# Optimization experiments

Hardware: AMD Instinct MI355X
Metric: run time of the kernel (lower is better)

## Reference

```python
import jax, jax.numpy as jnp
import numpy as np

D_MODEL = 768
MIMO_RANK = 4


def setup_inputs() -> dict:
    key = jax.random.key(0)
    ks = jax.random.split(key, 6)
    B, T, D, R = 2, 2048, D_MODEL, MIMO_RANK
    x = jax.random.normal(ks[0], (B, T, D), dtype=jnp.float32)
    norm_w = jnp.ones((D,), dtype=jnp.float32)
    W_in = jax.random.normal(ks[1], (D * R * 2, D), dtype=jnp.float32) * 0.02
    W_out = jax.random.normal(ks[2], (D, D), dtype=jnp.float32) * 0.02
    a_param = jax.random.normal(ks[3], (D, R, 2), dtype=jnp.float32) * 0.12
    b_param = jax.random.normal(ks[4], (D, R, 2), dtype=jnp.float32) * 0.15
    c_param = jax.random.normal(ks[5], (D, R, 2), dtype=jnp.float32) * 0.15
    return {"x": x, "norm_w": norm_w, "W_in": W_in, "W_out": W_out,
            "a_param": a_param, "b_param": b_param, "c_param": c_param}


def reference(x, norm_w, W_in, W_out, a_param, b_param, c_param):
    B, T, D = x.shape
    R = a_param.shape[1]
    # RMSNorm
    xn = x * jax.lax.rsqrt(jnp.mean(x * x, axis=-1, keepdims=True) + 1e-6) * norm_w
    # in_proj -> interleaved complex MIMO input u: [B,T,D,R,2]
    u = (xn @ W_in.T).reshape(B, T, D, R, 2)
    # coefficients (tanh-bounded; |a| scaled by 0.97 for stability)
    a = jnp.tanh(a_param) * 0.97
    b = jnp.tanh(b_param)
    c = jnp.tanh(c_param)
    ac = jax.lax.complex(a[..., 0], a[..., 1])  # [D,R]
    bc = jax.lax.complex(b[..., 0], b[..., 1])
    cc = jax.lax.complex(c[..., 0], c[..., 1])
    uc = jax.lax.complex(u[..., 0], u[..., 1])  # [B,T,D,R]
    # linear complex recurrence s_t = a * s_{t-1} + b * u_t, zero init state,
    # parallelized with an associative scan over time.
    bu = bc[None, None] * uc
    A = jnp.broadcast_to(ac[None, None], bu.shape)

    def comb(l, r):
        return (l[0] * r[0], r[0] * l[1] + r[1])

    _, s = jax.lax.associative_scan(comb, (A, bu), axis=1)  # [B,T,D,R] complex
    # output mix: real part of c * h, summed over MIMO rank -> [B,T,D]
    y = jnp.real(cc[None, None] * s).sum(axis=-1)
    return y @ W_out.T
```

## Files before the change

kernel.cpp:

```cpp
#include <hip/hip_runtime.h>
#include <hip/hip_bf16.h>
#include <stdint.h>

#define BATCH 2
#define TT 2048
#define DM 768
#define RR 4
#define M_TOK 4096
#define NFEAT 6144
#define NCH 6144
#define CHUNK 64
#define NCHUNK 32

typedef __attribute__((ext_vector_type(8))) short short8;
typedef __attribute__((ext_vector_type(4))) float float4v;

__device__ inline float bf2f(uint32_t bits16) {
    union { uint32_t u; float f; } x; x.u = bits16 << 16; return x.f;
}

typedef const __attribute__((address_space(1))) void* gptr_t;
typedef __attribute__((address_space(3))) void* lptr_t;

__device__ inline void async_ld16(const void* g, void* l) {
    __builtin_amdgcn_global_load_lds((gptr_t)(uintptr_t)g, (lptr_t)(uintptr_t)l,
                                     16, 0, 0);
}

__device__ inline void store_c(__hip_bfloat16* C, size_t idx, float v) {
    C[idx] = __float2bfloat16(v);
}
__device__ inline void store_c(float* C, size_t idx, float v) { C[idx] = v; }

__device__ inline uint2 pack4bf(float a, float b, float c, float d) {
    union { __hip_bfloat16 h[4]; uint2 u; } o;
    o.h[0] = __float2bfloat16(a); o.h[1] = __float2bfloat16(b);
    o.h[2] = __float2bfloat16(c); o.h[3] = __float2bfloat16(d);
    return o.u;
}

__device__ inline uint32_t pack2bf(float a, float b) {
    union { __hip_bfloat16 h[2]; uint32_t u; } o;
    o.h[0] = __float2bfloat16(a); o.h[1] = __float2bfloat16(b);
    return o.u;
}

__device__ inline float2 cmul(float2 a, float2 b) {
    return make_float2(a.x * b.x - a.y * b.y, a.x * b.y + a.y * b.x);
}

__device__ inline void cstep(float& sr, float& si, float2 a, float2 bb,
                             uint32_t uw) {
    float ur = bf2f(uw & 0xffffu), ui = bf2f(uw >> 16);
    float tr = bb.x * ur - bb.y * ui;
    float ti = bb.x * ui + bb.y * ur;
    float nr = a.x * sr - a.y * si + tr;
    float ni = a.x * si + a.y * sr + ti;
    sr = nr; si = ni;
}

__global__ __launch_bounds__(256) void prep_rms(
    const float* __restrict__ x, const float* __restrict__ w,
    const float* __restrict__ W_in, const float* __restrict__ W_out,
    const float* __restrict__ ap, const float* __restrict__ bp,
    const float* __restrict__ cp,
    __hip_bfloat16* __restrict__ xn,
    __hip_bfloat16* __restrict__ Win_bf, __hip_bfloat16* __restrict__ Wout_bf,
    float2* __restrict__ ac, float2* __restrict__ bc,
    float2* __restrict__ cc, float2* __restrict__ aQ,
    float2* __restrict__ aL) {
    int bid = blockIdx.x;
    int tid = threadIdx.x;
    if (bid < M_TOK) {
        __shared__ float wsum[3];
        float4 v = make_float4(0.f, 0.f, 0.f, 0.f);
        if (tid < 192) v = ((const float4*)(x + (size_t)bid * DM))[tid];
        float ss = v.x * v.x + v.y * v.y + v.z * v.z + v.w * v.w;
        #pragma unroll
        for (int o = 1; o < 64; o <<= 1) ss += __shfl_xor(ss, o);
        if (tid < 192 && (tid & 63) == 0) wsum[tid >> 6] = ss;
        __syncthreads();
        if (tid < 192) {
            float tot = wsum[0] + wsum[1] + wsum[2];
            float scale = rsqrtf(tot * (1.f / DM) + 1e-6f);
            float4 wv = ((const float4*)w)[tid];
            ((uint2*)(xn + (size_t)bid * DM))[tid] =
                pack4bf(v.x * scale * wv.x, v.y * scale * wv.y,
                        v.z * scale * wv.z, v.w * scale * wv.w);
        }
        return;
    }
    const int N1 = NFEAT * DM / 4;
    const int N2 = DM * DM / 4;
    int i = (bid - M_TOK) * 256 + tid;
    if (i < N1) {
        float4 v = ((const float4*)W_in)[i];
        ((uint2*)Win_bf)[i] = pack4bf(v.x, v.y, v.z, v.w);
    } else if (i < N1 + N2) {
        int k = i - N1;
        float4 v = ((const float4*)W_out)[k];
        ((uint2*)Wout_bf)[k] = pack4bf(v.x, v.y, v.z, v.w);
    }
    if (i < DM * RR) {
        float ar = tanhf(ap[2 * i])     * 0.97f;
        float ai = tanhf(ap[2 * i + 1]) * 0.97f;
        ac[i] = make_float2(ar, ai);
        bc[i] = make_float2(tanhf(bp[2 * i]), tanhf(bp[2 * i + 1]));
        cc[i] = make_float2(tanhf(cp[2 * i]), tanhf(cp[2 * i + 1]));
        float xr = ar, xi = ai;
        #pragma unroll
        for (int k = 0; k < 4; ++k) {
            float nr = xr * xr - xi * xi;
            float ni = 2.f * xr * xi;
            xr = nr; xi = ni;
        }
        aQ[i] = make_float2(xr, xi);
        #pragma unroll
        for (int k = 0; k < 2; ++k) {
            float nr = xr * xr - xi * xi;
            float ni = 2.f * xr * xi;
            xr = nr; xi = ni;
        }
        aL[i] = make_float2(xr, xi);
    }
}

template <int BM, int BN, int BK, typename OutT>
__device__ inline void gemm_body(
    const __hip_bfloat16* __restrict__ A, const __hip_bfloat16* __restrict__ B,
    OutT* __restrict__ C, int K, int ldc) {
    constexpr int MI = BM / 32;
    constexpr int NJ = BN / 32;
    constexpr int CPR = BK / 8;
    __shared__ __attribute__((aligned(16))) __hip_bfloat16 lA[BM * BK];
    __shared__ __attribute__((aligned(16))) __hip_bfloat16 lB[BN * BK];
    const int tid  = threadIdx.x;
    const int lane = tid & 63;
    const int wave = tid >> 6;
    const int quad = lane >> 4;
    const int l15  = lane & 15;
    const int wm = (wave >> 1) * (BM / 2);
    const int wn = (wave & 1) * (BN / 2);
    const int m0 = blockIdx.y * BM;
    const int n0 = blockIdx.x * BN;

    float4v acc[MI][NJ] = {};

    for (int k0 = 0; k0 < K; k0 += BK) {
        __syncthreads();
        #pragma unroll
        for (int it = 0; it < BM * CPR / 256; ++it) {
            int p = it * 256 + tid;
            int row = p / CPR;
            int cg = (p & (CPR - 1)) ^ (row & (CPR - 1));
            async_ld16(A + (size_t)(m0 + row) * K + k0 + cg * 8, lA + p * 8);
        }
        #pragma unroll
        for (int it = 0; it < BN * CPR / 256; ++it) {
            int p = it * 256 + tid;
            int row = p / CPR;
            int cg = (p & (CPR - 1)) ^ (row & (CPR - 1));
            async_ld16(B + (size_t)(n0 + row) * K + k0 + cg * 8, lB + p * 8);
        }
        __syncthreads();
        #pragma unroll
        for (int s = 0; s < BK / 32; ++s) {
            short8 af[MI], bfr[NJ];
            #pragma unroll
            for (int i = 0; i < MI; ++i) {
                int r = wm + i * 16 + l15;
                int c = (s * 4 + quad) ^ (r & (CPR - 1));
                af[i] = *(const short8*)(lA + r * BK + c * 8);
            }
            #pragma unroll
            for (int j = 0; j < NJ; ++j) {
                int r = wn + j * 16 + l15;
                int c = (s * 4 + quad) ^ (r & (CPR - 1));
                bfr[j] = *(const short8*)(lB + r * BK + c * 8);
            }
            #pragma unroll
            for (int i = 0; i < MI; ++i)
                #pragma unroll
                for (int j = 0; j < NJ; ++j)
                    acc[i][j] = __builtin_amdgcn_mfma_f32_16x16x32_bf16(
                        af[i], bfr[j], acc[i][j], 0, 0, 0);
        }
    }
    #pragma unroll
    for (int i = 0; i < MI; ++i)
        #pragma unroll
        for (int j = 0; j < NJ; ++j)
            #pragma unroll
            for (int rg = 0; rg < 4; ++rg) {
                int row = m0 + wm + i * 16 + quad * 4 + rg;
                int col = n0 + wn + j * 16 + l15;
                store_c(C, (size_t)row * ldc + col, acc[i][j][rg]);
            }
}

__global__ __launch_bounds__(256) void gemm_out(
    const __hip_bfloat16* __restrict__ A, const __hip_bfloat16* __restrict__ B,
    float* __restrict__ C, int K) {
    gemm_body<64, 64, 128, float>(A, B, C, K, DM);
}

__global__ __launch_bounds__(256) void gemm_in_scan(
    const __hip_bfloat16* __restrict__ A,
    const __hip_bfloat16* __restrict__ B,
    const float2* __restrict__ ac, const float2* __restrict__ bc,
    const float2* __restrict__ cc,
    __hip_bfloat16* __restrict__ y_local,
    float2* __restrict__ chunkEnd) {
    constexpr int BM = 128, BN = 128, BK = 64;
    constexpr int MI = BM / 32, NJ = BN / 32, CPR = BK / 8;
    constexpr int K = DM;
    __shared__ __attribute__((aligned(16))) __hip_bfloat16 smem[BM * BK + BN * BK];
    __hip_bfloat16* lA = smem;
    __hip_bfloat16* lB = smem + BM * BK;
    const int tid  = threadIdx.x;
    const int lane = tid & 63;
    const int wave = tid >> 6;
    const int quad = lane >> 4;
    const int l15  = lane & 15;
    const int wm = (wave >> 1) * (BM / 2);
    const int wn = (wave & 1) * (BN / 2);
    const int m0 = blockIdx.y * BM;
    const int n0 = blockIdx.x * BN;

    float4v acc[MI][NJ] = {};

    for (int k0 = 0; k0 < K; k0 += BK) {
        __syncthreads();
        #pragma unroll
        for (int it = 0; it < BM * CPR / 256; ++it) {
            int p = it * 256 + tid;
            int row = p / CPR;
            int cg = (p & (CPR - 1)) ^ (row & (CPR - 1));
            async_ld16(A + (size_t)(m0 + row) * K + k0 + cg * 8, lA + p * 8);
        }
        #pragma unroll
        for (int it = 0; it < BN * CPR / 256; ++it) {
            int p = it * 256 + tid;
            int row = p / CPR;
            int cg = (p & (CPR - 1)) ^ (row & (CPR - 1));
            async_ld16(B + (size_t)(n0 + row) * K + k0 + cg * 8, lB + p * 8);
        }
        __syncthreads();
        #pragma unroll
        for (int s = 0; s < BK / 32; ++s) {
            short8 af[MI], bfr[NJ];
            #pragma unroll
            for (int i = 0; i < MI; ++i) {
                int r = wm + i * 16 + l15;
                int c = (s * 4 + quad) ^ (r & (CPR - 1));
                af[i] = *(const short8*)(lA + r * BK + c * 8);
            }
            #pragma unroll
            for (int j = 0; j < NJ; ++j) {
                int r = wn + j * 16 + l15;
                int c = (s * 4 + quad) ^ (r & (CPR - 1));
                bfr[j] = *(const short8*)(lB + r * BK + c * 8);
            }
            #pragma unroll
            for (int i = 0; i < MI; ++i)
                #pragma unroll
                for (int j = 0; j < NJ; ++j)
                    acc[i][j] = __builtin_amdgcn_mfma_f32_16x16x32_bf16(
                        af[i], bfr[j], acc[i][j], 0, 0, 0);
        }
    }

    __syncthreads();
    uint32_t* up = (uint32_t*)smem;
    #pragma unroll
    for (int i = 0; i < MI; ++i)
        #pragma unroll
        for (int j = 0; j < NJ; ++j) {
            float s0 = __shfl_xor(acc[i][j][0], 1);
            float s1 = __shfl_xor(acc[i][j][1], 1);
            float s2 = __shfl_xor(acc[i][j][2], 1);
            float s3 = __shfl_xor(acc[i][j][3], 1);
            const bool odd = l15 & 1;
            float lo0 = odd ? s2 : acc[i][j][0];
            float hi0 = odd ? acc[i][j][2] : s0;
            float lo1 = odd ? s3 : acc[i][j][1];
            float hi1 = odd ? acc[i][j][3] : s1;
            int row0 = wm + i * 16 + quad * 4 + (odd ? 2 : 0);
            int row1 = row0 + 1;
            int pr = (wn + j * 16 + (l15 & ~1)) >> 1;
            int sl = pr & 3;
            up[row0 * 64 + (((pr >> 2) ^ (row0 & 15)) << 2) + sl] =
                pack2bf(lo0, hi0);
            up[row1 * 64 + (((pr >> 2) ^ (row1 & 15)) << 2) + sl] =
                pack2bf(lo1, hi1);
        }
    __syncthreads();

    if (tid < 32) {
        const int d_loc = tid & 15;
        const int half  = tid >> 4;
        const int d_g   = (n0 >> 3) + d_loc;
        const int cb    = d_g * RR;
        float2 a0 = ac[cb], a1 = ac[cb + 1], a2 = ac[cb + 2], a3 = ac[cb + 3];
        float2 b0 = bc[cb], b1 = bc[cb + 1], b2 = bc[cb + 2], b3 = bc[cb + 3];
        float2 c0 = cc[cb], c1 = cc[cb + 1], c2 = cc[cb + 2], c3 = cc[cb + 3];
        const int bb = m0 >> 11;
        const int j  = ((m0 & (TT - 1)) >> 6) + half;
        const uint4* up4 = (const uint4*)smem;
        float s0r = 0, s0i = 0, s1r = 0, s1i = 0;
        float s2r = 0, s2i = 0, s3r = 0, s3i = 0;
        size_t ybase = (size_t)(m0 + half * 64) * DM + d_g;
        #pragma unroll 4
        for (int t = 0; t < CHUNK; ++t) {
            int row = half * 64 + t;
            uint4 uw = up4[row * 16 + (d_loc ^ (row & 15))];
            cstep(s0r, s0i, a0, b0, uw.x);
            cstep(s1r, s1i, a1, b1, uw.y);
            cstep(s2r, s2i, a2, b2, uw.z);
            cstep(s3r, s3i, a3, b3, uw.w);
            float yv = c0.x * s0r - c0.y * s0i + c1.x * s1r - c1.y * s1i
                     + c2.x * s2r - c2.y * s2i + c3.x * s3r - c3.y * s3i;
            y_local[ybase + (size_t)t * DM] = __float2bfloat16(yv);
        }
        size_t eb = (size_t)j * NCH + bb * (DM * RR) + cb;
        chunkEnd[eb]     = make_float2(s0r, s0i);
        chunkEnd[eb + 1] = make_float2(s1r, s1i);
        chunkEnd[eb + 2] = make_float2(s2r, s2i);
        chunkEnd[eb + 3] = make_float2(s3r, s3i);
    }
}

__global__ __launch_bounds__(256) void scan_fix(
    const __hip_bfloat16* __restrict__ y_local,
    const float2* __restrict__ ac, const float2* __restrict__ cc,
    const float2* __restrict__ aQp, const float2* __restrict__ aLp,
    const float2* __restrict__ chunkEnd,
    __hip_bfloat16* __restrict__ y) {
    int g = blockIdx.x * 256 + threadIdx.x;
    int j = blockIdx.y;
    int z = blockIdx.z;
    int b = g >= DM;
    int d = g - b * DM;
    int cb = d * RR;
    float2 a0 = ac[cb], a1 = ac[cb + 1], a2 = ac[cb + 2], a3 = ac[cb + 3];
    float2 aL0 = aLp[cb], aL1 = aLp[cb + 1], aL2 = aLp[cb + 2], aL3 = aLp[cb + 3];
    float2 k0 = make_float2(0, 0), k1 = k0, k2 = k0, k3 = k0;
    for (int jj = 0; jj < j; ++jj) {
        size_t eb = (size_t)jj * NCH + b * (DM * RR) + cb;
        float2 e0 = chunkEnd[eb],     e1 = chunkEnd[eb + 1];
        float2 e2 = chunkEnd[eb + 2], e3 = chunkEnd[eb + 3];
        float nr, ni;
        nr = aL0.x * k0.x - aL0.y * k0.y + e0.x; ni = aL0.x * k0.y + aL0.y * k0.x + e0.y; k0 = make_float2(nr, ni);
        nr = aL1.x * k1.x - aL1.y * k1.y + e1.x; ni = aL1.x * k1.y + aL1.y * k1.x + e1.y; k1 = make_float2(nr, ni);
        nr = aL2.x * k2.x - aL2.y * k2.y + e2.x; ni = aL2.x * k2.y + aL2.y * k2.x + e2.y; k2 = make_float2(nr, ni);
        nr = aL3.x * k3.x - aL3.y * k3.y + e3.x; ni = aL3.x * k3.y + aL3.y * k3.x + e3.y; k3 = make_float2(nr, ni);
    }
    float2 q0 = cmul(cmul(cc[cb],     k0), a0);
    float2 q1 = cmul(cmul(cc[cb + 1], k1), a1);
    float2 q2 = cmul(cmul(cc[cb + 2], k2), a2);
    float2 q3 = cmul(cmul(cc[cb + 3], k3), a3);
    float2 aQ0 = aQp[cb], aQ1 = aQp[cb + 1], aQ2 = aQp[cb + 2], aQ3 = aQp[cb + 3];
    for (int zz = 0; zz < z; ++zz) {
        q0 = cmul(q0, aQ0); q1 = cmul(q1, aQ1);
        q2 = cmul(q2, aQ2); q3 = cmul(q3, aQ3);
    }
    size_t base = ((size_t)(b * TT + j * CHUNK + z * 16)) * DM + d;
    #pragma unroll 4
    for (int i = 0; i < 16; ++i) {
        float yv = bf2f(((const uint16_t*)y_local)[base + (size_t)i * DM])
                 + q0.x + q1.x + q2.x + q3.x;
        y[base + (size_t)i * DM] = __float2bfloat16(yv);
        q0 = cmul(q0, a0); q1 = cmul(q1, a1);
        q2 = cmul(q2, a2); q3 = cmul(q3, a3);
    }
}

extern "C" void kernel_launch(void* const* d_in, const int* in_sizes, int n_in,
                              void* d_out, int out_size, void* d_ws,
                              size_t ws_size, hipStream_t stream) {
    const float* x      = (const float*)d_in[0];
    const float* norm_w = (const float*)d_in[1];
    const float* W_in   = (const float*)d_in[2];
    const float* W_out  = (const float*)d_in[3];
    const float* a_p    = (const float*)d_in[4];
    const float* b_p    = (const float*)d_in[5];
    const float* c_p    = (const float*)d_in[6];
    float* out = (float*)d_out;

    char* ws = (char*)d_ws;
    size_t off = 0;
    auto alloc = [&](size_t bytes) {
        void* p = ws + off;
        off += (bytes + 255) & ~(size_t)255;
        return p;
    };
    __hip_bfloat16* Win_bf  = (__hip_bfloat16*)alloc((size_t)NFEAT * DM * 2);
    __hip_bfloat16* Wout_bf = (__hip_bfloat16*)alloc((size_t)DM * DM * 2);
    __hip_bfloat16* xn      = (__hip_bfloat16*)alloc((size_t)M_TOK * DM * 2);
    __hip_bfloat16* y_local = (__hip_bfloat16*)alloc((size_t)M_TOK * DM * 2);
    __hip_bfloat16* y       = (__hip_bfloat16*)alloc((size_t)M_TOK * DM * 2);
    float2* ac = (float2*)alloc((size_t)DM * RR * 8);
    float2* bc = (float2*)alloc((size_t)DM * RR * 8);
    float2* cc = (float2*)alloc((size_t)DM * RR * 8);
    float2* aQ = (float2*)alloc((size_t)DM * RR * 8);
    float2* aL = (float2*)alloc((size_t)DM * RR * 8);
    float2* chunkEnd = (float2*)alloc((size_t)NCHUNK * NCH * 8);

    {
        int cast_blocks = ((NFEAT * DM + DM * DM) / 4 + 255) / 256;
        prep_rms<<<M_TOK + cast_blocks, 256, 0, stream>>>(
            x, norm_w, W_in, W_out, a_p, b_p, c_p,
            xn, Win_bf, Wout_bf, ac, bc, cc, aQ, aL);
    }
    gemm_in_scan<<<dim3(NFEAT / 128, M_TOK / 128), 256, 0, stream>>>(
        xn, Win_bf, ac, bc, cc, y_local, chunkEnd);
    scan_fix<<<dim3(BATCH * DM / 256, NCHUNK, 4), 256, 0, stream>>>(
        y_local, ac, cc, aQ, aL, chunkEnd, y);
    gemm_out<<<dim3(DM / 64, M_TOK / 64), 256, 0, stream>>>(
        y, Wout_bf, out, DM);
}
```

Before: 198.7 us.

## Parallelize in-block chunk scan across all threads and pack RMSNorm per wave

The fused GEMM+scan epilogue previously ran the 64-step recurrence on only 32 threads. Now all 256 threads each scan 8 timesteps, exchange sub-chunk end states through extra shared memory, and combine them with a^8 carries before writing outputs. The LDS swizzle is changed to avoid bank conflicts for the new access pattern. RMSNorm now processes four tokens per block, one per wave, with no shared-memory reduction. The cost is extra LDS, another barrier, and a short serial carry loop per thread.

```diff
diff --git a/kernel.cpp b/kernel.cpp
--- a/kernel.cpp
+++ b/kernel.cpp
@@ -47,6 +47,13 @@
 
 __device__ inline float2 cmul(float2 a, float2 b) {
     return make_float2(a.x * b.x - a.y * b.y, a.x * b.y + a.y * b.x);
+}
+__device__ inline float2 cmad(float2 a, float2 b, float2 c) {
+    return make_float2(a.x * b.x - a.y * b.y + c.x,
+                       a.x * b.y + a.y * b.x + c.y);
+}
+__device__ inline float2 csq(float2 a) {
+    return make_float2(a.x * a.x - a.y * a.y, 2.f * a.x * a.y);
 }
 
 __device__ inline void cstep(float& sr, float& si, float2 a, float2 bb,
@@ -71,28 +78,32 @@
     float2* __restrict__ aL) {
     int bid = blockIdx.x;
     int tid = threadIdx.x;
-    if (bid < M_TOK) {
-        __shared__ float wsum[3];
-        float4 v = make_float4(0.f, 0.f, 0.f, 0.f);
-        if (tid < 192) v = ((const float4*)(x + (size_t)bid * DM))[tid];
-        float ss = v.x * v.x + v.y * v.y + v.z * v.z + v.w * v.w;
+    const int RMS_BLOCKS = M_TOK / 4;
+    if (bid < RMS_BLOCKS) {
+        int lane = tid & 63;
+        int token = bid * 4 + (tid >> 6);
+        const float4* xr = (const float4*)(x + (size_t)token * DM);
+        float4 v0 = xr[lane], v1 = xr[lane + 64], v2 = xr[lane + 128];
+        float ss = v0.x * v0.x + v0.y * v0.y + v0.z * v0.z + v0.w * v0.w
+                 + v1.x * v1.x + v1.y * v1.y + v1.z * v1.z + v1.w * v1.w
+                 + v2.x * v2.x + v2.y * v2.y + v2.z * v2.z + v2.w * v2.w;
         #pragma unroll
         for (int o = 1; o < 64; o <<= 1) ss += __shfl_xor(ss, o);
-        if (tid < 192 && (tid & 63) == 0) wsum[tid >> 6] = ss;
-        __syncthreads();
-        if (tid < 192) {
-            float tot = wsum[0] + wsum[1] + wsum[2];
-            float scale = rsqrtf(tot * (1.f / DM) + 1e-6f);
-            float4 wv = ((const float4*)w)[tid];
-            ((uint2*)(xn + (size_t)bid * DM))[tid] =
-                pack4bf(v.x * scale * wv.x, v.y * scale * wv.y,
-                        v.z * scale * wv.z, v.w * scale * wv.w);
-        }
+        float scale = rsqrtf(ss * (1.f / DM) + 1e-6f);
+        const float4* wr = (const float4*)w;
+        float4 w0 = wr[lane], w1 = wr[lane + 64], w2 = wr[lane + 128];
+        uint2* o = (uint2*)(xn + (size_t)token * DM);
+        o[lane] = pack4bf(v0.x * scale * w0.x, v0.y * scale * w0.y,
+                          v0.z * scale * w0.z, v0.w * scale * w0.w);
+        o[lane + 64] = pack4bf(v1.x * scale * w1.x, v1.y * scale * w1.y,
+                               v1.z * scale * w1.z, v1.w * scale * w1.w);
+        o[lane + 128] = pack4bf(v2.x * scale * w2.x, v2.y * scale * w2.y,
+                                v2.z * scale * w2.z, v2.w * scale * w2.w);
         return;
     }
     const int N1 = NFEAT * DM / 4;
     const int N2 = DM * DM / 4;
-    int i = (bid - M_TOK) * 256 + tid;
+    int i = (bid - RMS_BLOCKS) * 256 + tid;
     if (i < N1) {
         float4 v = ((const float4*)W_in)[i];
         ((uint2*)Win_bf)[i] = pack4bf(v.x, v.y, v.z, v.w);
@@ -214,7 +225,8 @@
     constexpr int BM = 128, BN = 128, BK = 64;
     constexpr int MI = BM / 32, NJ = BN / 32, CPR = BK / 8;
     constexpr int K = DM;
-    __shared__ __attribute__((aligned(16))) __hip_bfloat16 smem[BM * BK + BN * BK];
+    __shared__ __attribute__((aligned(16))) __hip_bfloat16
+        smem[BM * BK + BN * BK + 4096];
     __hip_bfloat16* lA = smem;
     __hip_bfloat16* lB = smem + BM * BK;
     const int tid  = threadIdx.x;
@@ -289,44 +301,78 @@
             int row1 = row0 + 1;
             int pr = (wn + j * 16 + (l15 & ~1)) >> 1;
             int sl = pr & 3;
-            up[row0 * 64 + (((pr >> 2) ^ (row0 & 15)) << 2) + sl] =
-                pack2bf(lo0, hi0);
-            up[row1 * 64 + (((pr >> 2) ^ (row1 & 15)) << 2) + sl] =
-                pack2bf(lo1, hi1);
+            int ch0 = (pr >> 2) ^ ((row0 ^ (row0 >> 2)) & 15);
+            int ch1 = (pr >> 2) ^ ((row1 ^ (row1 >> 2)) & 15);
+            up[row0 * 64 + ch0 * 4 + sl] = pack2bf(lo0, hi0);
+            up[row1 * 64 + ch1 * 4 + sl] = pack2bf(lo1, hi1);
         }
     __syncthreads();
 
-    if (tid < 32) {
+    {
         const int d_loc = tid & 15;
-        const int half  = tid >> 4;
+        const int s8    = (tid >> 4) & 7;
+        const int half  = tid >> 7;
         const int d_g   = (n0 >> 3) + d_loc;
         const int cb    = d_g * RR;
         float2 a0 = ac[cb], a1 = ac[cb + 1], a2 = ac[cb + 2], a3 = ac[cb + 3];
         float2 b0 = bc[cb], b1 = bc[cb + 1], b2 = bc[cb + 2], b3 = bc[cb + 3];
         float2 c0 = cc[cb], c1 = cc[cb + 1], c2 = cc[cb + 2], c3 = cc[cb + 3];
-        const int bb = m0 >> 11;
-        const int j  = ((m0 & (TT - 1)) >> 6) + half;
         const uint4* up4 = (const uint4*)smem;
+        float2* se = (float2*)(smem + (BM * BK + BN * BK));
+        const int rbase = half * 64 + s8 * 8;
+
         float s0r = 0, s0i = 0, s1r = 0, s1i = 0;
         float s2r = 0, s2i = 0, s3r = 0, s3i = 0;
-        size_t ybase = (size_t)(m0 + half * 64) * DM + d_g;
-        #pragma unroll 4
-        for (int t = 0; t < CHUNK; ++t) {
-            int row = half * 64 + t;
-            uint4 uw = up4[row * 16 + (d_loc ^ (row & 15))];
+        float yloc[8];
+        #pragma unroll
+        for (int i = 0; i < 8; ++i) {
+            int row = rbase + i;
+            uint4 uw = up4[row * 16 + (d_loc ^ ((row ^ (row >> 2)) & 15))];
             cstep(s0r, s0i, a0, b0, uw.x);
             cstep(s1r, s1i, a1, b1, uw.y);
             cstep(s2r, s2i, a2, b2, uw.z);
             cstep(s3r, s3i, a3, b3, uw.w);
-            float yv = c0.x * s0r - c0.y * s0i + c1.x * s1r - c1.y * s1i
-                     + c2.x * s2r - c2.y * s2i + c3.x * s3r - c3.y * s3i;
-            y_local[ybase + (size_t)t * DM] = __float2bfloat16(yv);
-        }
-        size_t eb = (size_t)j * NCH + bb * (DM * RR) + cb;
-        chunkEnd[eb]     = make_float2(s0r, s0i);
-        chunkEnd[eb + 1] = make_float2(s1r, s1i);
-        chunkEnd[eb + 2] = make_float2(s2r, s2i);
-        chunkEnd[eb + 3] = make_float2(s3r, s3i);
+            yloc[i] = c0.x * s0r - c0.y * s0i + c1.x * s1r - c1.y * s1i
+                    + c2.x * s2r - c2.y * s2i + c3.x * s3r - c3.y * s3i;
+        }
+        const int sbase = ((half * 8 + s8) * 16 + d_loc) * 4;
+        se[sbase]     = make_float2(s0r, s0i);
+        se[sbase + 1] = make_float2(s1r, s1i);
+        se[sbase + 2] = make_float2(s2r, s2i);
+        se[sbase + 3] = make_float2(s3r, s3i);
+        __syncthreads();
+
+        float2 aE0 = csq(csq(csq(a0))), aE1 = csq(csq(csq(a1)));
+        float2 aE2 = csq(csq(csq(a2))), aE3 = csq(csq(csq(a3)));
+        float2 C0 = make_float2(0, 0), C1 = C0, C2 = C0, C3 = C0;
+        for (int k = 0; k < s8; ++k) {
+            int kb = ((half * 8 + k) * 16 + d_loc) * 4;
+            C0 = cmad(C0, aE0, se[kb]);
+            C1 = cmad(C1, aE1, se[kb + 1]);
+            C2 = cmad(C2, aE2, se[kb + 2]);
+            C3 = cmad(C3, aE3, se[kb + 3]);
+        }
+        if (s8 == 7) {
+            const int bb = m0 >> 11;
+            const int j  = ((m0 & (TT - 1)) >> 6) + half;
+            size_t eb = (size_t)j * NCH + bb * (DM * RR) + cb;
+            chunkEnd[eb]     = cmad(C0, aE0, make_float2(s0r, s0i));
+            chunkEnd[eb + 1] = cmad(C1, aE1, make_float2(s1r, s1i));
+            chunkEnd[eb + 2] = cmad(C2, aE2, make_float2(s2r, s2i));
+            chunkEnd[eb + 3] = cmad(C3, aE3, make_float2(s3r, s3i));
+        }
+        float2 q0 = cmul(cmul(c0, C0), a0);
+        float2 q1 = cmul(cmul(c1, C1), a1);
+        float2 q2 = cmul(cmul(c2, C2), a2);
+        float2 q3 = cmul(cmul(c3, C3), a3);
+        size_t ybase = (size_t)(m0 + rbase) * DM + d_g;
+        #pragma unroll
+        for (int i = 0; i < 8; ++i) {
+            float yv = yloc[i] + q0.x + q1.x + q2.x + q3.x;
+            y_local[ybase + (size_t)i * DM] = __float2bfloat16(yv);
+            q0 = cmul(q0, a0); q1 = cmul(q1, a1);
+            q2 = cmul(q2, a2); q3 = cmul(q3, a3);
+        }
     }
 }
 
@@ -349,11 +395,8 @@
         size_t eb = (size_t)jj * NCH + b * (DM * RR) + cb;
         float2 e0 = chunkEnd[eb],     e1 = chunkEnd[eb + 1];
         float2 e2 = chunkEnd[eb + 2], e3 = chunkEnd[eb + 3];
-        float nr, ni;
-        nr = aL0.x * k0.x - aL0.y * k0.y + e0.x; ni = aL0.x * k0.y + aL0.y * k0.x + e0.y; k0 = make_float2(nr, ni);
-        nr = aL1.x * k1.x - aL1.y * k1.y + e1.x; ni = aL1.x * k1.y + aL1.y * k1.x + e1.y; k1 = make_float2(nr, ni);
-        nr = aL2.x * k2.x - aL2.y * k2.y + e2.x; ni = aL2.x * k2.y + aL2.y * k2.x + e2.y; k2 = make_float2(nr, ni);
-        nr = aL3.x * k3.x - aL3.y * k3.y + e3.x; ni = aL3.x * k3.y + aL3.y * k3.x + e3.y; k3 = make_float2(nr, ni);
+        k0 = cmad(k0, aL0, e0); k1 = cmad(k1, aL1, e1);
+        k2 = cmad(k2, aL2, e2); k3 = cmad(k3, aL3, e3);
     }
     float2 q0 = cmul(cmul(cc[cb],     k0), a0);
     float2 q1 = cmul(cmul(cc[cb + 1], k1), a1);
@@ -408,7 +451,7 @@
 
     {
         int cast_blocks = ((NFEAT * DM + DM * DM) / 4 + 255) / 256;
-        prep_rms<<<M_TOK + cast_blocks, 256, 0, stream>>>(
+        prep_rms<<<M_TOK / 4 + cast_blocks, 256, 0, stream>>>(
             x, norm_w, W_in, W_out, a_p, b_p, c_p,
             xn, Win_bf, Wout_bf, ac, bc, cc, aQ, aL);
     }
```

New measurement: 221.2 us. +11.3%, slower.
